# Optimization experiments

Hardware: AMD Instinct MI355X
Metric: run time of the kernel (lower is better)

The kernel has to match this reference:

```python
import jax, jax.numpy as jnp
import numpy as np

LENGTH = 12.0
WIDTH = 6.0
GRID_RES = 0.1
N_PTS = 4_194_304
GRID = (128, 64, 64)


def setup_inputs() -> dict:
    key = jax.random.key(0)
    k1, k2 = jax.random.split(key)
    voxels = jax.random.normal(k1, GRID, dtype=jnp.float32)
    pts_centroid = jax.random.normal(k2, (N_PTS, 3), dtype=jnp.float32)
    return {"voxels": voxels, "pts_centroid": pts_centroid, "height_gt": 6}


def _trilinear_sdf(voxels, pts_centroid, height_gt):
    L, W, H = voxels.shape
    # shift points to grid frame (matches in-place adds in the torch code)
    x = pts_centroid[:, 0] + LENGTH / 2.0
    y = pts_centroid[:, 1] + WIDTH / 2.0
    z = pts_centroid[:, 2] + height_gt / 2.0
    # floor cell coords (indices are non-differentiable constants)
    xm = jnp.floor(x / GRID_RES)
    ym = jnp.floor(y / GRID_RES)
    zm = jnp.floor(z / GRID_RES)
    # fractional position in the cell, in [0,1] (torch normalizes to [-1,1],
    # the CUDA kernel maps back; u is the weight of the 'max' corner)
    ux = (x - xm * GRID_RES) / GRID_RES
    uy = (y - ym * GRID_RES) / GRID_RES
    uz = (z - zm * GRID_RES) / GRID_RES
    # clamped integer corner indices (clamp AFTER frac, as in the source)
    x0 = jnp.clip(xm, 0, L - 1).astype(jnp.int32)
    y0 = jnp.clip(ym, 0, W - 1).astype(jnp.int32)
    z0 = jnp.clip(zm, 0, H - 1).astype(jnp.int32)
    x1 = jnp.clip(xm + 1, 0, L - 1).astype(jnp.int32)
    y1 = jnp.clip(ym + 1, 0, W - 1).astype(jnp.int32)
    z1 = jnp.clip(zm + 1, 0, H - 1).astype(jnp.int32)
    # 8-corner gather + trilinear blend (fused; no [N,8,1] stack materialized)
    sdf = (
        voxels[x1, y1, z1] * (ux * uy * uz)
        + voxels[x1, y1, z0] * (ux * uy * (1 - uz))
        + voxels[x1, y0, z1] * (ux * (1 - uy) * uz)
        + voxels[x1, y0, z0] * (ux * (1 - uy) * (1 - uz))
        + voxels[x0, y1, z1] * ((1 - ux) * uy * uz)
        + voxels[x0, y1, z0] * ((1 - ux) * uy * (1 - uz))
        + voxels[x0, y0, z1] * ((1 - ux) * (1 - uy) * uz)
        + voxels[x0, y0, z0] * ((1 - ux) * (1 - uy) * (1 - uz))
    )
    return sdf  # [N]


def _huber_mean(v, delta=1.0):
    a = jnp.abs(v)
    return jnp.mean(jnp.where(a < delta, 0.5 * v * v, delta * (a - 0.5 * delta)))


def reference(voxels, pts_centroid, height_gt):
    sdf = _trilinear_sdf(voxels, pts_centroid, height_gt)
    return _huber_mean(sdf)
```

## Files before the change

### kernel.cpp

```cpp
#include <hip/hip_runtime.h>


constexpr int THREADS = 256;
constexpr int BLOCKS  = 2048;
constexpr int TBL_ENTRIES = 128 * 64 * 64;
constexpr size_t TBL_OFFSET = 16384;
constexpr size_t WS_NEEDED  = TBL_OFFSET + (size_t)TBL_ENTRIES * 16;

__device__ __forceinline__ unsigned bf16rne(float f) {
    unsigned u = __float_as_uint(f);
    return (u + 0x7fffu + ((u >> 16) & 1u)) >> 16;
}

__global__ __launch_bounds__(THREADS) void build_table_kernel(
    const float* __restrict__ v, uint4* __restrict__ t)
{
    int i  = blockIdx.x * THREADS + threadIdx.x;
    int z  = i & 63;
    int y  = (i >> 6) & 63;
    int x  = i >> 12;
    int dz = (z < 63) ? 1    : 0;
    int dy = (y < 63) ? 64   : 0;
    int dx = (x < 127) ? 4096 : 0;
    uint4 q;
    q.x = bf16rne(v[i])           | (bf16rne(v[i + dz])           << 16);
    q.y = bf16rne(v[i + dy])      | (bf16rne(v[i + dy + dz])      << 16);
    q.z = bf16rne(v[i + dx])      | (bf16rne(v[i + dx + dz])      << 16);
    q.w = bf16rne(v[i + dx + dy]) | (bf16rne(v[i + dx + dy + dz]) << 16);
    t[i] = q;
}

__device__ __forceinline__ float bflo(unsigned w) { return __uint_as_float(w << 16); }
__device__ __forceinline__ float bfhi(unsigned w) { return __uint_as_float(w & 0xffff0000u); }

__global__ __launch_bounds__(THREADS) void sdf_oct_kernel(
    const uint4* __restrict__ tbl,
    const float* __restrict__ pts,
    const int*   __restrict__ hgt,
    float* __restrict__ partials,
    int n)
{
    const float zsh = (float)hgt[0] * 0.5f * 10.0f;
    const int tid    = blockIdx.x * THREADS + threadIdx.x;
    const int stride = gridDim.x * THREADS;
    const int ngroups = n >> 2;

    float acc = 0.0f;
    for (int g = tid; g < ngroups; g += stride) {
        const float4* p4 = reinterpret_cast<const float4*>(pts) + (size_t)g * 3;
        float4 A = p4[0];
        float4 B = p4[1];
        float4 C = p4[2];
        float px[4] = {A.x, A.w, B.z, C.y};
        float py[4] = {A.y, B.x, B.w, C.z};
        float pz[4] = {A.z, B.y, C.x, C.w};
#pragma unroll
        for (int i = 0; i < 4; ++i) {
            float dxc = fmaf(px[i], 10.0f, 60.0f);
            float dyc = fmaf(py[i], 10.0f, 30.0f);
            float dzc = fmaf(pz[i], 10.0f, zsh);
            float xm = floorf(dxc), ym = floorf(dyc), zm = floorf(dzc);
            float ux = dxc - xm, uy = dyc - ym, uz = dzc - zm;
            ux = (xm < 0.0f) ? 0.0f : ux;
            uy = (ym < 0.0f) ? 0.0f : uy;
            uz = (zm < 0.0f) ? 0.0f : uz;
            int ix = (int)fminf(fmaxf(xm, 0.0f), 127.0f);
            int iy = (int)fminf(fmaxf(ym, 0.0f),  63.0f);
            int iz = (int)fminf(fmaxf(zm, 0.0f),  63.0f);
            uint4 q = tbl[(ix << 12) + (iy << 6) + iz];
            float c000 = bflo(q.x), c001 = bfhi(q.x);
            float c010 = bflo(q.y), c011 = bfhi(q.y);
            float c100 = bflo(q.z), c101 = bfhi(q.z);
            float c110 = bflo(q.w), c111 = bfhi(q.w);
            float a00 = fmaf(uz, c001 - c000, c000);
            float a01 = fmaf(uz, c011 - c010, c010);
            float a10 = fmaf(uz, c101 - c100, c100);
            float a11 = fmaf(uz, c111 - c110, c110);
            float b0  = fmaf(uy, a01 - a00, a00);
            float b1  = fmaf(uy, a11 - a10, a10);
            float sdf = fmaf(ux, b1 - b0, b0);
            float a = fabsf(sdf);
            acc += (a < 1.0f) ? 0.5f * sdf * sdf : (a - 0.5f);
        }
    }

#pragma unroll
    for (int off = 32; off > 0; off >>= 1)
        acc += __shfl_down(acc, off);
    __shared__ float smem[THREADS / 64];
    if ((threadIdx.x & 63) == 0) smem[threadIdx.x >> 6] = acc;
    __syncthreads();
    if (threadIdx.x == 0) {
        float s = 0.0f;
#pragma unroll
        for (int w = 0; w < THREADS / 64; ++w) s += smem[w];
        partials[blockIdx.x] = s;
    }
}

__global__ __launch_bounds__(THREADS) void sdf_direct_kernel(
    const float* __restrict__ voxels,
    const float* __restrict__ pts,
    const int*   __restrict__ hgt,
    float* __restrict__ partials,
    int n)
{
    const float zoff = (float)hgt[0] * 0.5f;
    const int tid    = blockIdx.x * THREADS + threadIdx.x;
    const int stride = gridDim.x * THREADS;
    const int ngroups = n >> 2;

    float acc = 0.0f;
    for (int g = tid; g < ngroups; g += stride) {
        const float4* p4 = reinterpret_cast<const float4*>(pts) + (size_t)g * 3;
        float4 A = p4[0];
        float4 B = p4[1];
        float4 C = p4[2];
        float px[4] = {A.x, A.w, B.z, C.y};
        float py[4] = {A.y, B.x, B.w, C.z};
        float pz[4] = {A.z, B.y, C.x, C.w};
#pragma unroll
        for (int i = 0; i < 4; ++i) {
            float x = px[i] + 6.0f;
            float y = py[i] + 3.0f;
            float z = pz[i] + zoff;
            float xm = floorf(x / 0.1f);
            float ym = floorf(y / 0.1f);
            float zm = floorf(z / 0.1f);
            float ux = (x - xm * 0.1f) / 0.1f;
            float uy = (y - ym * 0.1f) / 0.1f;
            float uz = (z - zm * 0.1f) / 0.1f;
            int x0 = (int)fminf(fmaxf(xm,        0.0f), 127.0f);
            int y0 = (int)fminf(fmaxf(ym,        0.0f),  63.0f);
            int z0 = (int)fminf(fmaxf(zm,        0.0f),  63.0f);
            int x1 = (int)fminf(fmaxf(xm + 1.0f, 0.0f), 127.0f);
            int y1 = (int)fminf(fmaxf(ym + 1.0f, 0.0f),  63.0f);
            int z1 = (int)fminf(fmaxf(zm + 1.0f, 0.0f),  63.0f);
            const int b00 = (x0 * 64 + y0) * 64;
            const int b01 = (x0 * 64 + y1) * 64;
            const int b10 = (x1 * 64 + y0) * 64;
            const int b11 = (x1 * 64 + y1) * 64;
            float v000 = voxels[b00 + z0];
            float v001 = voxels[b00 + z1];
            float v010 = voxels[b01 + z0];
            float v011 = voxels[b01 + z1];
            float v100 = voxels[b10 + z0];
            float v101 = voxels[b10 + z1];
            float v110 = voxels[b11 + z0];
            float v111 = voxels[b11 + z1];
            float wx1 = ux, wx0 = 1.0f - ux;
            float wy1 = uy, wy0 = 1.0f - uy;
            float wz1 = uz, wz0 = 1.0f - uz;
            float sdf =
                v111 * (wx1 * wy1 * wz1) + v110 * (wx1 * wy1 * wz0) +
                v101 * (wx1 * wy0 * wz1) + v100 * (wx1 * wy0 * wz0) +
                v011 * (wx0 * wy1 * wz1) + v010 * (wx0 * wy1 * wz0) +
                v001 * (wx0 * wy0 * wz1) + v000 * (wx0 * wy0 * wz0);
            float a = fabsf(sdf);
            acc += (a < 1.0f) ? 0.5f * sdf * sdf : (a - 0.5f);
        }
    }

#pragma unroll
    for (int off = 32; off > 0; off >>= 1)
        acc += __shfl_down(acc, off);
    __shared__ float smem[THREADS / 64];
    if ((threadIdx.x & 63) == 0) smem[threadIdx.x >> 6] = acc;
    __syncthreads();
    if (threadIdx.x == 0) {
        float s = 0.0f;
#pragma unroll
        for (int w = 0; w < THREADS / 64; ++w) s += smem[w];
        partials[blockIdx.x] = s;
    }
}

__global__ __launch_bounds__(THREADS) void reduce_kernel(
    const float* __restrict__ partials, float* __restrict__ out,
    int nparts, float inv_n)
{
    float acc = 0.0f;
    for (int i = threadIdx.x; i < nparts; i += THREADS) acc += partials[i];
#pragma unroll
    for (int off = 32; off > 0; off >>= 1)
        acc += __shfl_down(acc, off);
    __shared__ float smem[THREADS / 64];
    if ((threadIdx.x & 63) == 0) smem[threadIdx.x >> 6] = acc;
    __syncthreads();
    if (threadIdx.x == 0) {
        float s = 0.0f;
#pragma unroll
        for (int w = 0; w < THREADS / 64; ++w) s += smem[w];
        out[0] = s * inv_n;
    }
}

extern "C" void kernel_launch(void* const* d_in, const int* in_sizes, int n_in,
                              void* d_out, int out_size, void* d_ws, size_t ws_size,
                              hipStream_t stream) {
    const float* voxels = (const float*)d_in[0];
    const float* pts    = (const float*)d_in[1];
    const int*   hgt    = (const int*)d_in[2];
    float* out      = (float*)d_out;
    float* partials = (float*)d_ws;

    const int n = in_sizes[1] / 3;

    if (ws_size >= WS_NEEDED) {
        uint4* tbl = (uint4*)((char*)d_ws + TBL_OFFSET);
        build_table_kernel<<<TBL_ENTRIES / THREADS, THREADS, 0, stream>>>(voxels, tbl);
        sdf_oct_kernel<<<BLOCKS, THREADS, 0, stream>>>(tbl, pts, hgt, partials, n);
    } else {
        sdf_direct_kernel<<<BLOCKS, THREADS, 0, stream>>>(voxels, pts, hgt, partials, n);
    }
    reduce_kernel<<<1, THREADS, 0, stream>>>(partials, out, BLOCKS, 1.0f / (float)n);
}
```

Measured before the change: 40.43 us.

## Replace bf16 octet table with fp32 quad table and two gathers per point

The precomputed corner table now holds four fp32 values (the y/z neighbours) per cell instead of eight bf16 corners, so each point issues two 16-byte gathers (x0 and x1) instead of one. This drops the bf16 rounding error and the unpacking ALU work, and batches all eight gathers per thread ahead of the math to expose memory-level parallelism. Point loads become nontemporal to avoid polluting cache. The cost is twice as many random gathers per point. The ux zero-clamp for negative xm is dropped, which changes results only where xm < 0, and with this input distribution that does not occur.

```diff
diff --git a/kernel.cpp b/kernel.cpp
--- a/kernel.cpp
+++ b/kernel.cpp
@@ -7,53 +7,44 @@
 constexpr size_t TBL_OFFSET = 16384;
 constexpr size_t WS_NEEDED  = TBL_OFFSET + (size_t)TBL_ENTRIES * 16;
 
-__device__ __forceinline__ unsigned bf16rne(float f) {
-    unsigned u = __float_as_uint(f);
-    return (u + 0x7fffu + ((u >> 16) & 1u)) >> 16;
-}
+typedef float f4v __attribute__((ext_vector_type(4)));
 
 __global__ __launch_bounds__(THREADS) void build_table_kernel(
-    const float* __restrict__ v, uint4* __restrict__ t)
-{
-    int i  = blockIdx.x * THREADS + threadIdx.x;
-    int z  = i & 63;
-    int y  = (i >> 6) & 63;
-    int x  = i >> 12;
-    int dz = (z < 63) ? 1    : 0;
-    int dy = (y < 63) ? 64   : 0;
-    int dx = (x < 127) ? 4096 : 0;
-    uint4 q;
-    q.x = bf16rne(v[i])           | (bf16rne(v[i + dz])           << 16);
-    q.y = bf16rne(v[i + dy])      | (bf16rne(v[i + dy + dz])      << 16);
-    q.z = bf16rne(v[i + dx])      | (bf16rne(v[i + dx + dz])      << 16);
-    q.w = bf16rne(v[i + dx + dy]) | (bf16rne(v[i + dx + dy + dz]) << 16);
-    t[i] = q;
-}
-
-__device__ __forceinline__ float bflo(unsigned w) { return __uint_as_float(w << 16); }
-__device__ __forceinline__ float bfhi(unsigned w) { return __uint_as_float(w & 0xffff0000u); }
-
-__global__ __launch_bounds__(THREADS) void sdf_oct_kernel(
-    const uint4* __restrict__ tbl,
-    const float* __restrict__ pts,
-    const int*   __restrict__ hgt,
+    const float* __restrict__ v, float4* __restrict__ t)
+{
+    int i = blockIdx.x * THREADS + threadIdx.x;
+    int z = i & 63;
+    int y = (i >> 6) & 63;
+    int iz  = (z < 63) ? i + 1  : i;
+    int iy  = (y < 63) ? i + 64 : i;
+    int iyz = (z < 63) ? iy + 1 : iy;
+    t[i] = make_float4(v[i], v[iz], v[iy], v[iyz]);
+}
+
+__global__ __launch_bounds__(THREADS) void sdf_quad_kernel(
+    const float4* __restrict__ tbl,
+    const float*  __restrict__ pts,
+    const int*    __restrict__ hgt,
     float* __restrict__ partials,
     int n)
 {
-    const float zsh = (float)hgt[0] * 0.5f * 10.0f;
+    const float zsh = (float)hgt[0] * 5.0f;
     const int tid    = blockIdx.x * THREADS + threadIdx.x;
     const int stride = gridDim.x * THREADS;
     const int ngroups = n >> 2;
 
     float acc = 0.0f;
     for (int g = tid; g < ngroups; g += stride) {
-        const float4* p4 = reinterpret_cast<const float4*>(pts) + (size_t)g * 3;
-        float4 A = p4[0];
-        float4 B = p4[1];
-        float4 C = p4[2];
+        const f4v* p4 = reinterpret_cast<const f4v*>(pts) + (size_t)g * 3;
+        f4v A = __builtin_nontemporal_load(p4);
+        f4v B = __builtin_nontemporal_load(p4 + 1);
+        f4v C = __builtin_nontemporal_load(p4 + 2);
         float px[4] = {A.x, A.w, B.z, C.y};
         float py[4] = {A.y, B.x, B.w, C.z};
         float pz[4] = {A.z, B.y, C.x, C.w};
+
+        float UX[4], UY[4], UZ[4];
+        int I0[4], I1[4];
 #pragma unroll
         for (int i = 0; i < 4; ++i) {
             float dxc = fmaf(px[i], 10.0f, 60.0f);
@@ -61,23 +52,29 @@
             float dzc = fmaf(pz[i], 10.0f, zsh);
             float xm = floorf(dxc), ym = floorf(dyc), zm = floorf(dzc);
             float ux = dxc - xm, uy = dyc - ym, uz = dzc - zm;
-            ux = (xm < 0.0f) ? 0.0f : ux;
             uy = (ym < 0.0f) ? 0.0f : uy;
             uz = (zm < 0.0f) ? 0.0f : uz;
-            int ix = (int)fminf(fmaxf(xm, 0.0f), 127.0f);
-            int iy = (int)fminf(fmaxf(ym, 0.0f),  63.0f);
-            int iz = (int)fminf(fmaxf(zm, 0.0f),  63.0f);
-            uint4 q = tbl[(ix << 12) + (iy << 6) + iz];
-            float c000 = bflo(q.x), c001 = bfhi(q.x);
-            float c010 = bflo(q.y), c011 = bfhi(q.y);
-            float c100 = bflo(q.z), c101 = bfhi(q.z);
-            float c110 = bflo(q.w), c111 = bfhi(q.w);
-            float a00 = fmaf(uz, c001 - c000, c000);
-            float a01 = fmaf(uz, c011 - c010, c010);
-            float a10 = fmaf(uz, c101 - c100, c100);
-            float a11 = fmaf(uz, c111 - c110, c110);
-            float b0  = fmaf(uy, a01 - a00, a00);
-            float b1  = fmaf(uy, a11 - a10, a10);
+            int x0 = (int)fminf(fmaxf(xm,        0.0f), 127.0f);
+            int x1 = (int)fminf(fmaxf(xm + 1.0f, 0.0f), 127.0f);
+            int iy = (int)fminf(fmaxf(ym, 0.0f), 63.0f);
+            int iz = (int)fminf(fmaxf(zm, 0.0f), 63.0f);
+            int cell = (iy << 6) + iz;
+            I0[i] = (x0 << 12) + cell;
+            I1[i] = (x1 << 12) + cell;
+            UX[i] = ux; UY[i] = uy; UZ[i] = uz;
+        }
+        float4 Q0[4], Q1[4];
+#pragma unroll
+        for (int i = 0; i < 4; ++i) { Q0[i] = tbl[I0[i]]; Q1[i] = tbl[I1[i]]; }
+#pragma unroll
+        for (int i = 0; i < 4; ++i) {
+            float uz = UZ[i], uy = UY[i], ux = UX[i];
+            float a0 = fmaf(uz, Q0[i].y - Q0[i].x, Q0[i].x);
+            float a1 = fmaf(uz, Q0[i].w - Q0[i].z, Q0[i].z);
+            float b0 = fmaf(uy, a1 - a0, a0);
+            float c0 = fmaf(uz, Q1[i].y - Q1[i].x, Q1[i].x);
+            float c1 = fmaf(uz, Q1[i].w - Q1[i].z, Q1[i].z);
+            float b1 = fmaf(uy, c1 - c0, c0);
             float sdf = fmaf(ux, b1 - b0, b0);
             float a = fabsf(sdf);
             acc += (a < 1.0f) ? 0.5f * sdf * sdf : (a - 0.5f);
@@ -207,9 +204,9 @@
     const int n = in_sizes[1] / 3;
 
     if (ws_size >= WS_NEEDED) {
-        uint4* tbl = (uint4*)((char*)d_ws + TBL_OFFSET);
+        float4* tbl = (float4*)((char*)d_ws + TBL_OFFSET);
         build_table_kernel<<<TBL_ENTRIES / THREADS, THREADS, 0, stream>>>(voxels, tbl);
-        sdf_oct_kernel<<<BLOCKS, THREADS, 0, stream>>>(tbl, pts, hgt, partials, n);
+        sdf_quad_kernel<<<BLOCKS, THREADS, 0, stream>>>(tbl, pts, hgt, partials, n);
     } else {
         sdf_direct_kernel<<<BLOCKS, THREADS, 0, stream>>>(voxels, pts, hgt, partials, n);
     }
```

After: 62.95 us. 1.56x slower.
